# Kernel tuning notes

Measured on AMD Instinct MI355X. Metric: run time of the kernel, lower is better.

Reference implementation:

```python
import jax, jax.numpy as jnp
import numpy as np

B, N, D, Y = 4, 2048, 512, 8921


def setup_inputs() -> dict:
    key = jax.random.key(0)
    ks = jax.random.split(key, 9)
    scale = 1.0 / np.sqrt(D)
    return {
        "x": jax.random.normal(ks[0], (B, N, D), jnp.float32),
        "target": (jax.random.uniform(ks[1], (B, Y), jnp.float32) > 0.98).astype(jnp.float32),
        "y_flow": jax.random.normal(ks[2], (B, Y), jnp.float32),
        "U_w": jax.random.normal(ks[3], (Y, D), jnp.float32) * scale,
        "Ug_w": jax.random.normal(ks[4], (Y, D), jnp.float32) * scale,
        "final_w": jax.random.normal(ks[5], (Y, D), jnp.float32) * scale,
        "final_b": jax.random.normal(ks[6], (Y,), jnp.float32) * scale,
        "gate_w": jax.random.normal(ks[7], (D,), jnp.float32) * scale,
        "gate_b": jax.random.normal(ks[8], (), jnp.float32) * scale,
    }


def reference(x, target, y_flow, U_w, Ug_w, final_w, final_b, gate_w, gate_b):
    # Label attention branch: alpha = softmax(U_w @ x^T) over tokens -> [B, Y, N]
    alpha = jax.nn.softmax(jnp.einsum("yd,bnd->byn", U_w, x), axis=-1)
    m = jnp.einsum("byn,bnd->byd", alpha, x)  # [B, Y, D]

    # Gate attention branch
    alpha_g = jax.nn.softmax(jnp.einsum("yd,bnd->byn", Ug_w, x), axis=-1)
    m_g = jnp.einsum("byn,bnd->byd", alpha_g, x)  # [B, Y, D]

    # gate = tanh(Linear(D,1)(m_gate)) -> [B, Y]
    gate = jnp.tanh(jnp.einsum("byd,d->by", m_g, gate_w) + gate_b)

    # y = sum_d(final_w * m) + final_b + y_flow * gate
    y = jnp.einsum("yd,byd->by", final_w, m) + final_b + y_flow * gate

    # BCEWithLogitsLoss (mean): logaddexp(0, y) - y * target, numerically stable
    loss = jnp.mean(jnp.logaddexp(0.0, y) - y * target)
    return (y, loss)
```

## Files before the change

### kernel.cpp

```cpp
#include <hip/hip_runtime.h>
#include <stdint.h>

#define BQ 4
#define NQ 2048
#define DQ 512
#define YQ 8921
#define YGRP 140
#define NH 4
#define NCHQ 32
#define NUNITS (YGRP * BQ * NH)
#define NLP 140
#define GXOFF 65536
#define L2E 1.44269504088896340736f

typedef __attribute__((ext_vector_type(8))) short bf16x8;
typedef __attribute__((ext_vector_type(4))) float f32x4;

__device__ inline short f2bf(float f) {
  unsigned u = __float_as_uint(f);
  u += 0x7fffu + ((u >> 16) & 1u);
  return (short)(u >> 16);
}

__device__ inline bf16x8 pack8(float4 a, float4 b) {
  bf16x8 h;
  h[0] = f2bf(a.x); h[1] = f2bf(a.y); h[2] = f2bf(a.z); h[3] = f2bf(a.w);
  h[4] = f2bf(b.x); h[5] = f2bf(b.y); h[6] = f2bf(b.z); h[7] = f2bf(b.w);
  return h;
}

__device__ inline void gl_lds16(const void* g, void* l) {
  __builtin_amdgcn_global_load_lds((const __attribute__((address_space(1))) void*)g,
                                   (__attribute__((address_space(3))) void*)l, 16, 0, 0);
}

__global__ __launch_bounds__(256) void prep_gx(const float* __restrict__ x,
                                               const float* __restrict__ gate_w,
                                               float* __restrict__ gx) {
  int rid = blockIdx.x * 4 + (threadIdx.x >> 6);
  int lane = threadIdx.x & 63;
  const float* src = x + (size_t)rid * DQ + lane * 8;
  float4 v0 = *(const float4*)src;
  float4 v1 = *(const float4*)(src + 4);
  const float* gwp = gate_w + lane * 8;
  float s = v0.x * gwp[0] + v0.y * gwp[1] + v0.z * gwp[2] + v0.w * gwp[3]
          + v1.x * gwp[4] + v1.y * gwp[5] + v1.z * gwp[6] + v1.w * gwp[7];
#pragma unroll
  for (int d = 1; d < 64; d <<= 1) s += __shfl_xor(s, d);
  if (lane == 0) gx[rid] = s;
}

__global__ __launch_bounds__(256) void prep_xfrag(const float* __restrict__ x,
                                                  const float* __restrict__ gate_w,
                                                  char* __restrict__ ws_x2,
                                                  float* __restrict__ gx) {
  __shared__ float xs[16 * 512];
  int t = blockIdx.x;
  const float* src = x + ((size_t)t << 13);
  int tid = threadIdx.x;
#pragma unroll
  for (int i = 0; i < 8; ++i)
    *(float4*)(xs + i * 1024 + tid * 4) = *(const float4*)(src + i * 1024 + tid * 4);
  __syncthreads();
  char* dst = ws_x2 + ((size_t)t << 14);
#pragma unroll
  for (int i = 0; i < 4; ++i) {
    int s = i * 256 + tid;
    int l = s & 63, kk = s >> 6;
    int row = l & 15, g = l >> 4;
    const float* p = xs + row * 512 + kk * 32 + g * 8;
    *(bf16x8*)(dst + s * 16) = pack8(*(const float4*)p, *(const float4*)(p + 4));
  }
  int row = tid >> 4, sub = tid & 15;
  const float* xr = xs + row * 512 + sub * 32;
  const float* gw = gate_w + sub * 32;
  float s = 0.f;
#pragma unroll
  for (int i = 0; i < 8; ++i) {
    float4 a = *(const float4*)(xr + i * 4);
    float4 g = *(const float4*)(gw + i * 4);
    s += a.x * g.x + a.y * g.y + a.z * g.z + a.w * g.w;
  }
  s += __shfl_xor(s, 1); s += __shfl_xor(s, 2);
  s += __shfl_xor(s, 4); s += __shfl_xor(s, 8);
  if (sub == 0) gx[t * 16 + row] = s;
}

__global__ __launch_bounds__(256) void prep_w(const float* __restrict__ Uw,
                                              const float* __restrict__ Gw,
                                              const float* __restrict__ Fw,
                                              char* __restrict__ ws_w) {
  int rid = blockIdx.x * 4 + (threadIdx.x >> 6);
  if (rid >= 3 * YQ) return;
  int lane = threadIdx.x & 63;
  int mat = rid / YQ, y = rid % YQ;
  const float* src = (mat == 0 ? Uw : (mat == 1 ? Gw : Fw)) + (size_t)y * DQ + lane * 8;
  *(bf16x8*)(ws_w + (size_t)rid * 1024 + lane * 16) =
      pack8(*(const float4*)src, *(const float4*)(src + 4));
}

template<bool FULL>
__global__ __launch_bounds__(256, 2) void fused_kernel(
    const float* __restrict__ x, const char* __restrict__ ws_x2,
    const char* __restrict__ ws_w,
    const float* __restrict__ Uw, const float* __restrict__ Gw,
    const float* __restrict__ Fw, const float* __restrict__ gx,
    float4* __restrict__ ws_state) {
  extern __shared__ char smem[];
  const int tid = threadIdx.x, l = tid & 63, w = tid >> 6;
  const int lr = l & 15, lg4 = l >> 4;
  int u = (blockIdx.x & 7) * (NUNITS / 8) + (blockIdx.x >> 3);
  const int b = u / (YGRP * NH);
  const int r0 = u % (YGRP * NH);
  const int yg = r0 / NH, nh = r0 % NH;
  const int ybase = yg * 64 + w * 16;
  const int nbase = nh * (NQ / NH);

  bf16x8 wU[16], wG[16], wF[16];
  {
    int y = ybase + lr; if (y >= YQ) y = YQ - 1;
    if constexpr (FULL) {
      const char* p0 = ws_w + ((size_t)y * DQ + lg4 * 8) * 2;
#pragma unroll
      for (int kk = 0; kk < 16; ++kk) {
        wU[kk] = *(const bf16x8*)(p0 + kk * 64);
        wG[kk] = *(const bf16x8*)(p0 + (size_t)YQ * 1024 + kk * 64);
        wF[kk] = *(const bf16x8*)(p0 + (size_t)YQ * 2048 + kk * 64);
      }
    } else {
      const float* pu = Uw + (size_t)y * DQ + lg4 * 8;
      const float* pg = Gw + (size_t)y * DQ + lg4 * 8;
      const float* pf = Fw + (size_t)y * DQ + lg4 * 8;
#pragma unroll
      for (int kk = 0; kk < 16; ++kk) {
        wU[kk] = pack8(*(const float4*)(pu + kk * 32), *(const float4*)(pu + kk * 32 + 4));
        wG[kk] = pack8(*(const float4*)(pg + kk * 32), *(const float4*)(pg + kk * 32 + 4));
        wF[kk] = pack8(*(const float4*)(pf + kk * 32), *(const float4*)(pf + kk * 32 + 4));
      }
    }
  }

  float lU = 0.f, aU = 0.f, lG = 0.f, aG = 0.f;

  if constexpr (FULL) {
    *(float2*)(smem + GXOFF + tid * 8) = *(const float2*)(gx + b * NQ + nbase + tid * 2);
    const char* xb = ws_x2 + (((size_t)(b * 128 + nh * 32)) << 14);
    auto stage = [&](int c) {
      const char* src = xb + ((size_t)c << 14);
      char* lb = smem + (c & 3) * 16384;
#pragma unroll
      for (int j = 0; j < 4; ++j) {
        int s = w * 4 + j;
        gl_lds16(src + s * 1024 + l * 16, lb + s * 1024);
      }
    };
    auto mfma_only = [&](int c, f32x4& sU, f32x4& sG, f32x4& sF) {
      const char* ab = smem + (c & 3) * 16384 + l * 16;
#pragma unroll
      for (int r = 0; r < 4; ++r) { sU[r] = 0.f; sG[r] = 0.f; sF[r] = 0.f; }
      __builtin_amdgcn_s_setprio(1);
#pragma unroll
      for (int kk = 0; kk < 16; ++kk) {
        bf16x8 a = *(const bf16x8*)(ab + kk * 1024);
        sU = __builtin_amdgcn_mfma_f32_16x16x32_bf16(a, wU[kk], sU, 0, 0, 0);
        sG = __builtin_amdgcn_mfma_f32_16x16x32_bf16(a, wG[kk], sG, 0, 0, 0);
        sF = __builtin_amdgcn_mfma_f32_16x16x32_bf16(a, wF[kk], sF, 0, 0, 0);
      }
      __builtin_amdgcn_s_setprio(0);
    };
    auto tail = [&](int c, const f32x4& sU, const f32x4& sG, const f32x4& sF) {
      float4 gxv = *(const float4*)(smem + GXOFF + c * 64 + lg4 * 16);
      float gv[4] = {gxv.x, gxv.y, gxv.z, gxv.w};
#pragma unroll
      for (int r = 0; r < 4; ++r) {
        float eu = __builtin_amdgcn_exp2f(sU[r] * L2E);
        lU += eu; aU = fmaf(eu, sF[r], aU);
        float eg = __builtin_amdgcn_exp2f(sG[r] * L2E);
        lG += eg; aG = fmaf(eg, gv[r], aG);
      }
    };

    __syncthreads();
    stage(0); stage(1);
    asm volatile("s_waitcnt vmcnt(4)" ::: "memory");
    __builtin_amdgcn_s_barrier();

    f32x4 pU, pG, pF, qU, qG, qF;
    mfma_only(0, pU, pG, pF);

#pragma unroll 1
    for (int cp = 0; cp < 15; ++cp) {
      const int c0 = 2 * cp;
      stage(c0 + 2); stage(c0 + 3);
      asm volatile("s_waitcnt vmcnt(8)" ::: "memory");
      __builtin_amdgcn_sched_barrier(0);
      __builtin_amdgcn_s_barrier();
      mfma_only(c0 + 1, qU, qG, qF);
      tail(c0, pU, pG, pF);
      asm volatile("s_waitcnt vmcnt(4)" ::: "memory");
      __builtin_amdgcn_sched_barrier(0);
      __builtin_amdgcn_s_barrier();
      mfma_only(c0 + 2, pU, pG, pF);
      tail(c0 + 1, qU, qG, qF);
    }
    asm volatile("s_waitcnt vmcnt(0)" ::: "memory");
    __builtin_amdgcn_sched_barrier(0);
    __builtin_amdgcn_s_barrier();
    mfma_only(31, qU, qG, qF);
    tail(30, pU, pG, pF);
    tail(31, qU, qG, qF);
  } else {
    const float* gxb = gx + b * NQ + nbase + lg4 * 4;
    for (int c = 0; c < NCHQ; ++c) {
      __syncthreads();
#pragma unroll
      for (int j = 0; j < 4; ++j) {
        int slot = j * 256 + tid;
        int kk = slot >> 6, l2 = slot & 63;
        int row = l2 & 15, g4 = l2 >> 4;
        const float* g = x + ((size_t)(b * NQ + nbase + c * 16 + row)) * DQ
                       + kk * 32 + g4 * 8;
        *(bf16x8*)(smem + slot * 16) = pack8(*(const float4*)g, *(const float4*)(g + 4));
      }
      __syncthreads();
      const char* ab = smem + l * 16;
      f32x4 sU = {0.f, 0.f, 0.f, 0.f}, sG = sU, sF = sU;
#pragma unroll
      for (int kk = 0; kk < 16; ++kk) {
        bf16x8 a = *(const bf16x8*)(ab + kk * 1024);
        sU = __builtin_amdgcn_mfma_f32_16x16x32_bf16(a, wU[kk], sU, 0, 0, 0);
        sG = __builtin_amdgcn_mfma_f32_16x16x32_bf16(a, wG[kk], sG, 0, 0, 0);
        sF = __builtin_amdgcn_mfma_f32_16x16x32_bf16(a, wF[kk], sF, 0, 0, 0);
      }
      float4 gxv = *(const float4*)(gxb + c * 16);
      float gv[4] = {gxv.x, gxv.y, gxv.z, gxv.w};
#pragma unroll
      for (int r = 0; r < 4; ++r) {
        float eu = __builtin_amdgcn_exp2f(sU[r] * L2E);
        lU += eu; aU = fmaf(eu, sF[r], aU);
        float eg = __builtin_amdgcn_exp2f(sG[r] * L2E);
        lG += eg; aG = fmaf(eg, gv[r], aG);
      }
    }
  }

#pragma unroll
  for (int d = 16; d < 64; d <<= 1) {
    lU += __shfl_xor(lU, d); aU += __shfl_xor(aU, d);
    lG += __shfl_xor(lG, d); aG += __shfl_xor(aG, d);
  }

  int y = ybase + lr;
  if (lg4 == 0 && y < YQ) {
    float4 st; st.x = lU; st.y = aU; st.z = lG; st.w = aG;
    ws_state[(size_t)(b * NH + nh) * YQ + y] = st;
  }
}

__global__ __launch_bounds__(256) void merge_kernel(
    const float4* __restrict__ ws_state, const float* __restrict__ fb,
    const float* __restrict__ gate_b, const float* __restrict__ yflow,
    const float* __restrict__ target, float* __restrict__ out_y,
    float* __restrict__ loss_part) {
  __shared__ float sb[256];
  int t = blockIdx.x * 256 + threadIdx.x;
  float lt = 0.f;
  if (t < BQ * YQ) {
    int b = t / YQ, y = t % YQ;
    float lU = 0.f, aU = 0.f, lG = 0.f, aG = 0.f;
#pragma unroll
    for (int nh = 0; nh < NH; ++nh) {
      float4 s = ws_state[(size_t)(b * NH + nh) * YQ + y];
      lU += s.x; aU += s.y; lG += s.z; aG += s.w;
    }
    float gate = tanhf(aG / lG + gate_b[0]);
    float yv = aU / lU + fb[y] + yflow[t] * gate;
    out_y[t] = yv;
    float tg = target[t];
    lt = fmaxf(yv, 0.f) + log1pf(__expf(-fabsf(yv))) - yv * tg;
  }
  sb[threadIdx.x] = lt;
  __syncthreads();
  for (int st = 128; st > 0; st >>= 1) {
    if (threadIdx.x < st) sb[threadIdx.x] += sb[threadIdx.x + st];
    __syncthreads();
  }
  if (threadIdx.x == 0) loss_part[blockIdx.x] = sb[0];
}

__global__ __launch_bounds__(256) void loss_kernel(const float* __restrict__ lp,
                                                   float* __restrict__ out) {
  __shared__ float sb[256];
  float s = (threadIdx.x < NLP) ? lp[threadIdx.x] : 0.f;
  sb[threadIdx.x] = s;
  __syncthreads();
  for (int st = 128; st > 0; st >>= 1) {
    if (threadIdx.x < st) sb[threadIdx.x] += sb[threadIdx.x + st];
    __syncthreads();
  }
  if (threadIdx.x == 0) out[BQ * YQ] = sb[0] / (float)(BQ * YQ);
}

extern "C" void kernel_launch(void* const* d_in, const int* in_sizes, int n_in,
                              void* d_out, int out_size, void* d_ws, size_t ws_size,
                              hipStream_t stream) {
  const float* x      = (const float*)d_in[0];
  const float* target = (const float*)d_in[1];
  const float* yflow  = (const float*)d_in[2];
  const float* Uw     = (const float*)d_in[3];
  const float* Gw     = (const float*)d_in[4];
  const float* Fw     = (const float*)d_in[5];
  const float* fb     = (const float*)d_in[6];
  const float* gw     = (const float*)d_in[7];
  const float* gb     = (const float*)d_in[8];
  float* out = (float*)d_out;
  char* ws = (char*)d_ws;

  const size_t xbytes  = (size_t)BQ * NQ * DQ * 2;
  const size_t wbytes  = (size_t)3 * YQ * DQ * 2;
  const size_t gxbytes = (size_t)BQ * NQ * 4;
  const size_t stbytes = (size_t)BQ * NH * YQ * 16;
  const size_t lpbytes = (size_t)NLP * 4;
  const bool full = ws_size >= xbytes + wbytes + gxbytes + stbytes + lpbytes;

  char* ws_x2; char* ws_w; float* gxp; float4* stp; float* lp;
  if (full) {
    ws_x2 = ws; ws_w = ws + xbytes;
    gxp = (float*)(ws + xbytes + wbytes);
    stp = (float4*)(ws + xbytes + wbytes + gxbytes);
    lp  = (float*)(ws + xbytes + wbytes + gxbytes + stbytes);
  } else {
    ws_x2 = nullptr; ws_w = nullptr;
    gxp = (float*)ws;
    stp = (float4*)(ws + gxbytes);
    lp  = (float*)(ws + gxbytes + stbytes);
  }

  (void)hipFuncSetAttribute(reinterpret_cast<const void*>(&fused_kernel<true>),
                            hipFuncAttributeMaxDynamicSharedMemorySize, 67584);
  (void)hipFuncSetAttribute(reinterpret_cast<const void*>(&fused_kernel<false>),
                            hipFuncAttributeMaxDynamicSharedMemorySize, 16384);

  if (full) {
    prep_xfrag<<<dim3(BQ * 128), 256, 0, stream>>>(x, gw, ws_x2, gxp);
    prep_w<<<dim3((3 * YQ + 3) / 4), 256, 0, stream>>>(Uw, Gw, Fw, ws_w);
    fused_kernel<true ><<<dim3(NUNITS), 256, 67584, stream>>>(
        x, ws_x2, ws_w, Uw, Gw, Fw, gxp, stp);
  } else {
    prep_gx<<<dim3(2048), 256, 0, stream>>>(x, gw, gxp);
    fused_kernel<false><<<dim3(NUNITS), 256, 16384, stream>>>(
        x, ws_x2, ws_w, Uw, Gw, Fw, gxp, stp);
  }
  merge_kernel<<<dim3(NLP), 256, 0, stream>>>(stp, fb, gb, yflow, target, out, lp);
  loss_kernel<<<1, 256, 0, stream>>>(lp, out);
}
```

Before: 219.7 us.

## Split chunk MFMA into quarter phases with register double-buffered LDS reads, merge prep kernels

The main loop now processes each 16-token chunk in four k-quarters, holding LDS fragments in two register buffers so the reads for the next quarter overlap the current MFMAs. Global-to-LDS staging is spread one slice per quarter with finer waitcnt and barriers. The two prep kernels are merged into a single launch to save one kernel launch. In exchange the loop has more barriers per chunk and there is less overlap between the exp tail and the MFMAs, since tail now runs after the chunk's last MFMA instead of alongside the next chunk.

```diff
diff --git a/kernel.cpp b/kernel.cpp
--- a/kernel.cpp
+++ b/kernel.cpp
@@ -10,6 +10,7 @@
 #define NCHQ 32
 #define NUNITS (YGRP * BQ * NH)
 #define NLP 140
+#define NWB ((3 * YQ + 3) / 4)
 #define GXOFF 65536
 #define L2E 1.44269504088896340736f
 
@@ -50,53 +51,54 @@
   if (lane == 0) gx[rid] = s;
 }
 
-__global__ __launch_bounds__(256) void prep_xfrag(const float* __restrict__ x,
-                                                  const float* __restrict__ gate_w,
-                                                  char* __restrict__ ws_x2,
-                                                  float* __restrict__ gx) {
+__global__ __launch_bounds__(256) void prep_all(const float* __restrict__ x,
+                                                const float* __restrict__ gate_w,
+                                                const float* __restrict__ Uw,
+                                                const float* __restrict__ Gw,
+                                                const float* __restrict__ Fw,
+                                                char* __restrict__ ws_x2,
+                                                char* __restrict__ ws_w,
+                                                float* __restrict__ gx) {
   __shared__ float xs[16 * 512];
-  int t = blockIdx.x;
-  const float* src = x + ((size_t)t << 13);
   int tid = threadIdx.x;
-#pragma unroll
-  for (int i = 0; i < 8; ++i)
-    *(float4*)(xs + i * 1024 + tid * 4) = *(const float4*)(src + i * 1024 + tid * 4);
-  __syncthreads();
-  char* dst = ws_x2 + ((size_t)t << 14);
-#pragma unroll
-  for (int i = 0; i < 4; ++i) {
-    int s = i * 256 + tid;
-    int l = s & 63, kk = s >> 6;
-    int row = l & 15, g = l >> 4;
-    const float* p = xs + row * 512 + kk * 32 + g * 8;
-    *(bf16x8*)(dst + s * 16) = pack8(*(const float4*)p, *(const float4*)(p + 4));
-  }
-  int row = tid >> 4, sub = tid & 15;
-  const float* xr = xs + row * 512 + sub * 32;
-  const float* gw = gate_w + sub * 32;
-  float s = 0.f;
-#pragma unroll
-  for (int i = 0; i < 8; ++i) {
-    float4 a = *(const float4*)(xr + i * 4);
-    float4 g = *(const float4*)(gw + i * 4);
-    s += a.x * g.x + a.y * g.y + a.z * g.z + a.w * g.w;
-  }
-  s += __shfl_xor(s, 1); s += __shfl_xor(s, 2);
-  s += __shfl_xor(s, 4); s += __shfl_xor(s, 8);
-  if (sub == 0) gx[t * 16 + row] = s;
-}
-
-__global__ __launch_bounds__(256) void prep_w(const float* __restrict__ Uw,
-                                              const float* __restrict__ Gw,
-                                              const float* __restrict__ Fw,
-                                              char* __restrict__ ws_w) {
-  int rid = blockIdx.x * 4 + (threadIdx.x >> 6);
-  if (rid >= 3 * YQ) return;
-  int lane = threadIdx.x & 63;
-  int mat = rid / YQ, y = rid % YQ;
-  const float* src = (mat == 0 ? Uw : (mat == 1 ? Gw : Fw)) + (size_t)y * DQ + lane * 8;
-  *(bf16x8*)(ws_w + (size_t)rid * 1024 + lane * 16) =
-      pack8(*(const float4*)src, *(const float4*)(src + 4));
+  if (blockIdx.x < 512) {
+    int t = blockIdx.x;
+    const float* src = x + ((size_t)t << 13);
+#pragma unroll
+    for (int i = 0; i < 8; ++i)
+      *(float4*)(xs + i * 1024 + tid * 4) = *(const float4*)(src + i * 1024 + tid * 4);
+    __syncthreads();
+    char* dst = ws_x2 + ((size_t)t << 14);
+#pragma unroll
+    for (int i = 0; i < 4; ++i) {
+      int s = i * 256 + tid;
+      int l = s & 63, kk = s >> 6;
+      int row = l & 15, g = l >> 4;
+      const float* p = xs + row * 512 + kk * 32 + g * 8;
+      *(bf16x8*)(dst + s * 16) = pack8(*(const float4*)p, *(const float4*)(p + 4));
+    }
+    int row = tid >> 4, sub = tid & 15;
+    const float* xr = xs + row * 512 + sub * 32;
+    const float* gw = gate_w + sub * 32;
+    float s = 0.f;
+#pragma unroll
+    for (int i = 0; i < 8; ++i) {
+      float4 a = *(const float4*)(xr + i * 4);
+      float4 g = *(const float4*)(gw + i * 4);
+      s += a.x * g.x + a.y * g.y + a.z * g.z + a.w * g.w;
+    }
+    s += __shfl_xor(s, 1); s += __shfl_xor(s, 2);
+    s += __shfl_xor(s, 4); s += __shfl_xor(s, 8);
+    if (sub == 0) gx[t * 16 + row] = s;
+  } else {
+    int rid = (blockIdx.x - 512) * 4 + (tid >> 6);
+    if (rid >= 3 * YQ) return;
+    int lane = tid & 63;
+    int mat = rid / YQ, y = rid % YQ;
+    const float* src = (mat == 0 ? Uw : (mat == 1 ? Gw : Fw)) + (size_t)y * DQ + lane * 8;
+    *(bf16x8*)(ws_w + (size_t)rid * 1024 + lane * 16) =
+        pack8(*(const float4*)src, *(const float4*)(src + 4));
+  }
 }
 
 template<bool FULL>
@@ -145,30 +147,31 @@
   if constexpr (FULL) {
     *(float2*)(smem + GXOFF + tid * 8) = *(const float2*)(gx + b * NQ + nbase + tid * 2);
     const char* xb = ws_x2 + (((size_t)(b * 128 + nh * 32)) << 14);
-    auto stage = [&](int c) {
-      const char* src = xb + ((size_t)c << 14);
-      char* lb = smem + (c & 3) * 16384;
-#pragma unroll
-      for (int j = 0; j < 4; ++j) {
-        int s = w * 4 + j;
-        gl_lds16(src + s * 1024 + l * 16, lb + s * 1024);
-      }
+
+    f32x4 sU, sG, sF;
+    auto stage1 = [&](int c, int j) {
+      int s = w * 4 + j;
+      gl_lds16(xb + ((size_t)c << 14) + s * 1024 + l * 16,
+               smem + (c & 3) * 16384 + s * 1024);
     };
-    auto mfma_only = [&](int c, f32x4& sU, f32x4& sG, f32x4& sF) {
-      const char* ab = smem + (c & 3) * 16384 + l * 16;
-#pragma unroll
-      for (int r = 0; r < 4; ++r) { sU[r] = 0.f; sG[r] = 0.f; sF[r] = 0.f; }
+    auto read4 = [&](int c, int p, bf16x8* A) {
+      const char* ab = smem + (c & 3) * 16384 + p * 4096 + l * 16;
+      A[0] = *(const bf16x8*)(ab);
+      A[1] = *(const bf16x8*)(ab + 1024);
+      A[2] = *(const bf16x8*)(ab + 2048);
+      A[3] = *(const bf16x8*)(ab + 3072);
+    };
+    auto mfma12 = [&](const bf16x8* A, int p) {
       __builtin_amdgcn_s_setprio(1);
 #pragma unroll
-      for (int kk = 0; kk < 16; ++kk) {
-        bf16x8 a = *(const bf16x8*)(ab + kk * 1024);
-        sU = __builtin_amdgcn_mfma_f32_16x16x32_bf16(a, wU[kk], sU, 0, 0, 0);
-        sG = __builtin_amdgcn_mfma_f32_16x16x32_bf16(a, wG[kk], sG, 0, 0, 0);
-        sF = __builtin_amdgcn_mfma_f32_16x16x32_bf16(a, wF[kk], sF, 0, 0, 0);
+      for (int kk = 0; kk < 4; ++kk) {
+        sU = __builtin_amdgcn_mfma_f32_16x16x32_bf16(A[kk], wU[p * 4 + kk], sU, 0, 0, 0);
+        sG = __builtin_amdgcn_mfma_f32_16x16x32_bf16(A[kk], wG[p * 4 + kk], sG, 0, 0, 0);
+        sF = __builtin_amdgcn_mfma_f32_16x16x32_bf16(A[kk], wF[p * 4 + kk], sF, 0, 0, 0);
       }
       __builtin_amdgcn_s_setprio(0);
     };
-    auto tail = [&](int c, const f32x4& sU, const f32x4& sG, const f32x4& sF) {
+    auto tail = [&](int c) {
       float4 gxv = *(const float4*)(smem + GXOFF + c * 64 + lg4 * 16);
       float gv[4] = {gxv.x, gxv.y, gxv.z, gxv.w};
 #pragma unroll
@@ -181,34 +184,49 @@
     };
 
     __syncthreads();
-    stage(0); stage(1);
+#pragma unroll
+    for (int j = 0; j < 4; ++j) stage1(0, j);
+#pragma unroll
+    for (int j = 0; j < 4; ++j) stage1(1, j);
     asm volatile("s_waitcnt vmcnt(4)" ::: "memory");
     __builtin_amdgcn_s_barrier();
 
-    f32x4 pU, pG, pF, qU, qG, qF;
-    mfma_only(0, pU, pG, pF);
+    bf16x8 Ra[4], Rb[4];
+    read4(0, 0, Ra);
 
 #pragma unroll 1
-    for (int cp = 0; cp < 15; ++cp) {
-      const int c0 = 2 * cp;
-      stage(c0 + 2); stage(c0 + 3);
-      asm volatile("s_waitcnt vmcnt(8)" ::: "memory");
+    for (int c = 0; c < NCHQ; ++c) {
+      const int cn = (c + 1 < NCHQ) ? c + 1 : c;
+      const bool st = (c + 2 < NCHQ);
+#pragma unroll
+      for (int r = 0; r < 4; ++r) { sU[r] = 0.f; sG[r] = 0.f; sF[r] = 0.f; }
+      read4(c, 1, Rb);
+      if (st) stage1(c + 2, 0);
+      __builtin_amdgcn_s_barrier();
       __builtin_amdgcn_sched_barrier(0);
+      mfma12(Ra, 0);
+      read4(c, 2, Ra);
+      if (st) stage1(c + 2, 1);
       __builtin_amdgcn_s_barrier();
-      mfma_only(c0 + 1, qU, qG, qF);
-      tail(c0, pU, pG, pF);
-      asm volatile("s_waitcnt vmcnt(4)" ::: "memory");
       __builtin_amdgcn_sched_barrier(0);
+      mfma12(Rb, 1);
+      read4(c, 3, Rb);
+      if (st) {
+        stage1(c + 2, 2);
+        asm volatile("s_waitcnt vmcnt(3)" ::: "memory");
+      } else {
+        asm volatile("s_waitcnt vmcnt(0)" ::: "memory");
+      }
       __builtin_amdgcn_s_barrier();
-      mfma_only(c0 + 2, pU, pG, pF);
-      tail(c0 + 1, qU, qG, qF);
-    }
-    asm volatile("s_waitcnt vmcnt(0)" ::: "memory");
-    __builtin_amdgcn_sched_barrier(0);
-    __builtin_amdgcn_s_barrier();
-    mfma_only(31, qU, qG, qF);
-    tail(30, pU, pG, pF);
-    tail(31, qU, qG, qF);
+      __builtin_amdgcn_sched_barrier(0);
+      mfma12(Ra, 2);
+      read4(cn, 0, Ra);
+      if (st) stage1(c + 2, 3);
+      __builtin_amdgcn_s_barrier();
+      __builtin_amdgcn_sched_barrier(0);
+      mfma12(Rb, 3);
+      tail(c);
+    }
   } else {
     const float* gxb = gx + b * NQ + nbase + lg4 * 4;
     for (int c = 0; c < NCHQ; ++c) {
@@ -342,8 +360,7 @@
                             hipFuncAttributeMaxDynamicSharedMemorySize, 16384);
 
   if (full) {
-    prep_xfrag<<<dim3(BQ * 128), 256, 0, stream>>>(x, gw, ws_x2, gxp);
-    prep_w<<<dim3((3 * YQ + 3) / 4), 256, 0, stream>>>(Uw, Gw, Fw, ws_w);
+    prep_all<<<dim3(512 + NWB), 256, 0, stream>>>(x, gw, Uw, Gw, Fw, ws_x2, ws_w, gxp);
     fused_kernel<true ><<<dim3(NUNITS), 256, 67584, stream>>>(
         x, ws_x2, ws_w, Uw, Gw, Fw, gxp, stp);
   } else {
```

New measurement: 222.5 us. Within noise of the previous version (+1.3%).

## Split fused kernel into U/F and gate warp roles with 6 waves per block

Applied to the files above, without the earlier changes.

The fused attention kernel now runs 384 threads per block. Four waves hold U and F weight fragments and two waves hold G weights for 32 labels each, so each wave keeps two weight sets in registers instead of three. The software-pipelined 2-chunk loop becomes a simpler triple-buffered loop with one barrier per chunk, which also shrinks shared memory. The two prep kernels are merged into one launch, and the per-label state is split into two float2 arrays. Register pressure drops and more waves are resident, but the pipeline is simpler, there is one barrier per chunk, and work is uneven across wave roles.

```diff
diff --git a/kernel.cpp b/kernel.cpp
--- a/kernel.cpp
+++ b/kernel.cpp
@@ -10,7 +10,8 @@
 #define NCHQ 32
 #define NUNITS (YGRP * BQ * NH)
 #define NLP 140
-#define GXOFF 65536
+#define NWB ((3 * YQ + 3) / 4)
+#define GXOFF 49152
 #define L2E 1.44269504088896340736f
 
 typedef __attribute__((ext_vector_type(8))) short bf16x8;
@@ -50,62 +51,63 @@
   if (lane == 0) gx[rid] = s;
 }
 
-__global__ __launch_bounds__(256) void prep_xfrag(const float* __restrict__ x,
-                                                  const float* __restrict__ gate_w,
-                                                  char* __restrict__ ws_x2,
-                                                  float* __restrict__ gx) {
+__global__ __launch_bounds__(256) void prep_all(const float* __restrict__ x,
+                                                const float* __restrict__ gate_w,
+                                                const float* __restrict__ Uw,
+                                                const float* __restrict__ Gw,
+                                                const float* __restrict__ Fw,
+                                                char* __restrict__ ws_x2,
+                                                char* __restrict__ ws_w,
+                                                float* __restrict__ gx) {
   __shared__ float xs[16 * 512];
-  int t = blockIdx.x;
-  const float* src = x + ((size_t)t << 13);
   int tid = threadIdx.x;
-#pragma unroll
-  for (int i = 0; i < 8; ++i)
-    *(float4*)(xs + i * 1024 + tid * 4) = *(const float4*)(src + i * 1024 + tid * 4);
-  __syncthreads();
-  char* dst = ws_x2 + ((size_t)t << 14);
-#pragma unroll
-  for (int i = 0; i < 4; ++i) {
-    int s = i * 256 + tid;
-    int l = s & 63, kk = s >> 6;
-    int row = l & 15, g = l >> 4;
-    const float* p = xs + row * 512 + kk * 32 + g * 8;
-    *(bf16x8*)(dst + s * 16) = pack8(*(const float4*)p, *(const float4*)(p + 4));
-  }
-  int row = tid >> 4, sub = tid & 15;
-  const float* xr = xs + row * 512 + sub * 32;
-  const float* gw = gate_w + sub * 32;
-  float s = 0.f;
-#pragma unroll
-  for (int i = 0; i < 8; ++i) {
-    float4 a = *(const float4*)(xr + i * 4);
-    float4 g = *(const float4*)(gw + i * 4);
-    s += a.x * g.x + a.y * g.y + a.z * g.z + a.w * g.w;
-  }
-  s += __shfl_xor(s, 1); s += __shfl_xor(s, 2);
-  s += __shfl_xor(s, 4); s += __shfl_xor(s, 8);
-  if (sub == 0) gx[t * 16 + row] = s;
-}
-
-__global__ __launch_bounds__(256) void prep_w(const float* __restrict__ Uw,
-                                              const float* __restrict__ Gw,
-                                              const float* __restrict__ Fw,
-                                              char* __restrict__ ws_w) {
-  int rid = blockIdx.x * 4 + (threadIdx.x >> 6);
-  if (rid >= 3 * YQ) return;
-  int lane = threadIdx.x & 63;
-  int mat = rid / YQ, y = rid % YQ;
-  const float* src = (mat == 0 ? Uw : (mat == 1 ? Gw : Fw)) + (size_t)y * DQ + lane * 8;
-  *(bf16x8*)(ws_w + (size_t)rid * 1024 + lane * 16) =
-      pack8(*(const float4*)src, *(const float4*)(src + 4));
+  if (blockIdx.x < 512) {
+    int t = blockIdx.x;
+    const float* src = x + ((size_t)t << 13);
+#pragma unroll
+    for (int i = 0; i < 8; ++i)
+      *(float4*)(xs + i * 1024 + tid * 4) = *(const float4*)(src + i * 1024 + tid * 4);
+    __syncthreads();
+    char* dst = ws_x2 + ((size_t)t << 14);
+#pragma unroll
+    for (int i = 0; i < 4; ++i) {
+      int s = i * 256 + tid;
+      int l = s & 63, kk = s >> 6;
+      int row = l & 15, g = l >> 4;
+      const float* p = xs + row * 512 + kk * 32 + g * 8;
+      *(bf16x8*)(dst + s * 16) = pack8(*(const float4*)p, *(const float4*)(p + 4));
+    }
+    int row = tid >> 4, sub = tid & 15;
+    const float* xr = xs + row * 512 + sub * 32;
+    const float* gw = gate_w + sub * 32;
+    float s = 0.f;
+#pragma unroll
+    for (int i = 0; i < 8; ++i) {
+      float4 a = *(const float4*)(xr + i * 4);
+      float4 g = *(const float4*)(gw + i * 4);
+      s += a.x * g.x + a.y * g.y + a.z * g.z + a.w * g.w;
+    }
+    s += __shfl_xor(s, 1); s += __shfl_xor(s, 2);
+    s += __shfl_xor(s, 4); s += __shfl_xor(s, 8);
+    if (sub == 0) gx[t * 16 + row] = s;
+  } else {
+    int rid = (blockIdx.x - 512) * 4 + (tid >> 6);
+    if (rid >= 3 * YQ) return;
+    int lane = tid & 63;
+    int mat = rid / YQ, y = rid % YQ;
+    const float* src = (mat == 0 ? Uw : (mat == 1 ? Gw : Fw)) + (size_t)y * DQ + lane * 8;
+    *(bf16x8*)(ws_w + (size_t)rid * 1024 + lane * 16) =
+        pack8(*(const float4*)src, *(const float4*)(src + 4));
+  }
 }
 
 template<bool FULL>
-__global__ __launch_bounds__(256, 2) void fused_kernel(
+__global__ __launch_bounds__(384, 2) void fused_kernel(
     const float* __restrict__ x, const char* __restrict__ ws_x2,
     const char* __restrict__ ws_w,
     const float* __restrict__ Uw, const float* __restrict__ Gw,
     const float* __restrict__ Fw, const float* __restrict__ gx,
-    float4* __restrict__ ws_state) {
+    float2* __restrict__ stUF, float2* __restrict__ stG) {
   extern __shared__ char smem[];
   const int tid = threadIdx.x, l = tid & 63, w = tid >> 6;
   const int lr = l & 15, lg4 = l >> 4;
@@ -113,155 +115,168 @@
   const int b = u / (YGRP * NH);
   const int r0 = u % (YGRP * NH);
   const int yg = r0 / NH, nh = r0 % NH;
-  const int ybase = yg * 64 + w * 16;
   const int nbase = nh * (NQ / NH);
-
-  bf16x8 wU[16], wG[16], wF[16];
+  const bool isUF = (w < 4);
+  const int ya0 = yg * 64 + (isUF ? w * 16 : (w - 4) * 32);
+  const int yb0 = isUF ? ya0 : (ya0 + 16);
+
+  bf16x8 wA[16], wB[16];
   {
-    int y = ybase + lr; if (y >= YQ) y = YQ - 1;
+    int ya = ya0 + lr; if (ya >= YQ) ya = YQ - 1;
+    int yb = yb0 + lr; if (yb >= YQ) yb = YQ - 1;
     if constexpr (FULL) {
-      const char* p0 = ws_w + ((size_t)y * DQ + lg4 * 8) * 2;
+      const size_t yoff = (size_t)YQ * 1024;
+      const char* pa = ws_w + ((size_t)ya * DQ + lg4 * 8) * 2 + (isUF ? 0 : yoff);
+      const char* pb = ws_w + ((size_t)yb * DQ + lg4 * 8) * 2 + (isUF ? 2 * yoff : yoff);
 #pragma unroll
       for (int kk = 0; kk < 16; ++kk) {
-        wU[kk] = *(const bf16x8*)(p0 + kk * 64);
-        wG[kk] = *(const bf16x8*)(p0 + (size_t)YQ * 1024 + kk * 64);
-        wF[kk] = *(const bf16x8*)(p0 + (size_t)YQ * 2048 + kk * 64);
+        wA[kk] = *(const bf16x8*)(pa + kk * 64);
+        wB[kk] = *(const bf16x8*)(pb + kk * 64);
       }
     } else {
-      const float* pu = Uw + (size_t)y * DQ + lg4 * 8;
-      const float* pg = Gw + (size_t)y * DQ + lg4 * 8;
-      const float* pf = Fw + (size_t)y * DQ + lg4 * 8;
+      const float* pa = (isUF ? Uw : Gw) + (size_t)ya * DQ + lg4 * 8;
+      const float* pb = (isUF ? Fw : Gw) + (size_t)yb * DQ + lg4 * 8;
 #pragma unroll
       for (int kk = 0; kk < 16; ++kk) {
-        wU[kk] = pack8(*(const float4*)(pu + kk * 32), *(const float4*)(pu + kk * 32 + 4));
-        wG[kk] = pack8(*(const float4*)(pg + kk * 32), *(const float4*)(pg + kk * 32 + 4));
-        wF[kk] = pack8(*(const float4*)(pf + kk * 32), *(const float4*)(pf + kk * 32 + 4));
-      }
-    }
-  }
-
-  float lU = 0.f, aU = 0.f, lG = 0.f, aG = 0.f;
+        wA[kk] = pack8(*(const float4*)(pa + kk * 32), *(const float4*)(pa + kk * 32 + 4));
+        wB[kk] = pack8(*(const float4*)(pb + kk * 32), *(const float4*)(pb + kk * 32 + 4));
+      }
+    }
+  }
+
+  float l0 = 0.f, a0 = 0.f, l1 = 0.f, a1 = 0.f;
 
   if constexpr (FULL) {
-    *(float2*)(smem + GXOFF + tid * 8) = *(const float2*)(gx + b * NQ + nbase + tid * 2);
+    if (tid < 256)
+      *(float2*)(smem + GXOFF + tid * 8) = *(const float2*)(gx + b * NQ + nbase + tid * 2);
     const char* xb = ws_x2 + (((size_t)(b * 128 + nh * 32)) << 14);
     auto stage = [&](int c) {
       const char* src = xb + ((size_t)c << 14);
-      char* lb = smem + (c & 3) * 16384;
+      char* lb = smem + (c % 3) * 16384;
 #pragma unroll
       for (int j = 0; j < 4; ++j) {
         int s = w * 4 + j;
         gl_lds16(src + s * 1024 + l * 16, lb + s * 1024);
       }
     };
-    auto mfma_only = [&](int c, f32x4& sU, f32x4& sG, f32x4& sF) {
-      const char* ab = smem + (c & 3) * 16384 + l * 16;
-#pragma unroll
-      for (int r = 0; r < 4; ++r) { sU[r] = 0.f; sG[r] = 0.f; sF[r] = 0.f; }
+    auto compute = [&](int c) {
+      const char* ab = smem + (c % 3) * 16384 + l * 16;
+      f32x4 sA = {0.f, 0.f, 0.f, 0.f}, sB = sA;
       __builtin_amdgcn_s_setprio(1);
 #pragma unroll
       for (int kk = 0; kk < 16; ++kk) {
         bf16x8 a = *(const bf16x8*)(ab + kk * 1024);
-        sU = __builtin_amdgcn_mfma_f32_16x16x32_bf16(a, wU[kk], sU, 0, 0, 0);
-        sG = __builtin_amdgcn_mfma_f32_16x16x32_bf16(a, wG[kk], sG, 0, 0, 0);
-        sF = __builtin_amdgcn_mfma_f32_16x16x32_bf16(a, wF[kk], sF, 0, 0, 0);
+        sA = __builtin_amdgcn_mfma_f32_16x16x32_bf16(a, wA[kk], sA, 0, 0, 0);
+        sB = __builtin_amdgcn_mfma_f32_16x16x32_bf16(a, wB[kk], sB, 0, 0, 0);
       }
       __builtin_amdgcn_s_setprio(0);
+      if (isUF) {
+#pragma unroll
+        for (int r = 0; r < 4; ++r) {
+          float e = __builtin_amdgcn_exp2f(sA[r] * L2E);
+          l0 += e; a0 = fmaf(e, sB[r], a0);
+        }
+      } else {
+        float4 gxv = *(const float4*)(smem + GXOFF + c * 64 + lg4 * 16);
+        float gv[4] = {gxv.x, gxv.y, gxv.z, gxv.w};
+#pragma unroll
+        for (int r = 0; r < 4; ++r) {
+          float ea = __builtin_amdgcn_exp2f(sA[r] * L2E);
+          l0 += ea; a0 = fmaf(ea, gv[r], a0);
+          float eb = __builtin_amdgcn_exp2f(sB[r] * L2E);
+          l1 += eb; a1 = fmaf(eb, gv[r], a1);
+        }
+      }
     };
-    auto tail = [&](int c, const f32x4& sU, const f32x4& sG, const f32x4& sF) {
-      float4 gxv = *(const float4*)(smem + GXOFF + c * 64 + lg4 * 16);
-      float gv[4] = {gxv.x, gxv.y, gxv.z, gxv.w};
-#pragma unroll
-      for (int r = 0; r < 4; ++r) {
-        float eu = __builtin_amdgcn_exp2f(sU[r] * L2E);
-        lU += eu; aU = fmaf(eu, sF[r], aU);
-        float eg = __builtin_amdgcn_exp2f(sG[r] * L2E);
-        lG += eg; aG = fmaf(eg, gv[r], aG);
-      }
-    };
 
     __syncthreads();
-    stage(0); stage(1);
-    asm volatile("s_waitcnt vmcnt(4)" ::: "memory");
+    if (isUF) {
+      stage(0); stage(1);
+      asm volatile("s_waitcnt vmcnt(4)" ::: "memory");
+    }
     __builtin_amdgcn_s_barrier();
 
-    f32x4 pU, pG, pF, qU, qG, qF;
-    mfma_only(0, pU, pG, pF);
-
 #pragma unroll 1
-    for (int cp = 0; cp < 15; ++cp) {
-      const int c0 = 2 * cp;
-      stage(c0 + 2); stage(c0 + 3);
-      asm volatile("s_waitcnt vmcnt(8)" ::: "memory");
-      __builtin_amdgcn_sched_barrier(0);
-      __builtin_amdgcn_s_barrier();
-      mfma_only(c0 + 1, qU, qG, qF);
-      tail(c0, pU, pG, pF);
-      asm volatile("s_waitcnt vmcnt(4)" ::: "memory");
-      __builtin_amdgcn_sched_barrier(0);
-      __builtin_amdgcn_s_barrier();
-      mfma_only(c0 + 2, pU, pG, pF);
-      tail(c0 + 1, qU, qG, qF);
-    }
-    asm volatile("s_waitcnt vmcnt(0)" ::: "memory");
-    __builtin_amdgcn_sched_barrier(0);
-    __builtin_amdgcn_s_barrier();
-    mfma_only(31, qU, qG, qF);
-    tail(30, pU, pG, pF);
-    tail(31, qU, qG, qF);
+    for (int c = 0; c < NCHQ; ++c) {
+      if (isUF && c + 2 < NCHQ) stage(c + 2);
+      compute(c);
+      if (isUF) {
+        if (c + 2 < NCHQ)      asm volatile("s_waitcnt vmcnt(4)" ::: "memory");
+        else if (c + 1 < NCHQ) asm volatile("s_waitcnt vmcnt(0)" ::: "memory");
+      }
+      if (c + 1 < NCHQ) {
+        __builtin_amdgcn_sched_barrier(0);
+        __builtin_amdgcn_s_barrier();
+      }
+    }
   } else {
     const float* gxb = gx + b * NQ + nbase + lg4 * 4;
     for (int c = 0; c < NCHQ; ++c) {
       __syncthreads();
 #pragma unroll
-      for (int j = 0; j < 4; ++j) {
-        int slot = j * 256 + tid;
-        int kk = slot >> 6, l2 = slot & 63;
-        int row = l2 & 15, g4 = l2 >> 4;
-        const float* g = x + ((size_t)(b * NQ + nbase + c * 16 + row)) * DQ
-                       + kk * 32 + g4 * 8;
-        *(bf16x8*)(smem + slot * 16) = pack8(*(const float4*)g, *(const float4*)(g + 4));
+      for (int i = 0; i < 3; ++i) {
+        int slot = i * 384 + tid;
+        if (slot < 1024) {
+          int kk = slot >> 6, l2 = slot & 63;
+          int row = l2 & 15, g4 = l2 >> 4;
+          const float* g = x + ((size_t)(b * NQ + nbase + c * 16 + row)) * DQ
+                         + kk * 32 + g4 * 8;
+          *(bf16x8*)(smem + slot * 16) = pack8(*(const float4*)g, *(const float4*)(g + 4));
+        }
       }
       __syncthreads();
       const char* ab = smem + l * 16;
-      f32x4 sU = {0.f, 0.f, 0.f, 0.f}, sG = sU, sF = sU;
+      f32x4 sA = {0.f, 0.f, 0.f, 0.f}, sB = sA;
 #pragma unroll
       for (int kk = 0; kk < 16; ++kk) {
         bf16x8 a = *(const bf16x8*)(ab + kk * 1024);
-        sU = __builtin_amdgcn_mfma_f32_16x16x32_bf16(a, wU[kk], sU, 0, 0, 0);
-        sG = __builtin_amdgcn_mfma_f32_16x16x32_bf16(a, wG[kk], sG, 0, 0, 0);
-        sF = __builtin_amdgcn_mfma_f32_16x16x32_bf16(a, wF[kk], sF, 0, 0, 0);
-      }
-      float4 gxv = *(const float4*)(gxb + c * 16);
-      float gv[4] = {gxv.x, gxv.y, gxv.z, gxv.w};
-#pragma unroll
-      for (int r = 0; r < 4; ++r) {
-        float eu = __builtin_amdgcn_exp2f(sU[r] * L2E);
-        lU += eu; aU = fmaf(eu, sF[r], aU);
-        float eg = __builtin_amdgcn_exp2f(sG[r] * L2E);
-        lG += eg; aG = fmaf(eg, gv[r], aG);
+        sA = __builtin_amdgcn_mfma_f32_16x16x32_bf16(a, wA[kk], sA, 0, 0, 0);
+        sB = __builtin_amdgcn_mfma_f32_16x16x32_bf16(a, wB[kk], sB, 0, 0, 0);
+      }
+      if (isUF) {
+#pragma unroll
+        for (int r = 0; r < 4; ++r) {
+          float e = __builtin_amdgcn_exp2f(sA[r] * L2E);
+          l0 += e; a0 = fmaf(e, sB[r], a0);
+        }
+      } else {
+        float4 gxv = *(const float4*)(gxb + c * 16);
+        float gv[4] = {gxv.x, gxv.y, gxv.z, gxv.w};
+#pragma unroll
+        for (int r = 0; r < 4; ++r) {
+          float ea = __builtin_amdgcn_exp2f(sA[r] * L2E);
+          l0 += ea; a0 = fmaf(ea, gv[r], a0);
+          float eb = __builtin_amdgcn_exp2f(sB[r] * L2E);
+          l1 += eb; a1 = fmaf(eb, gv[r], a1);
+        }
       }
     }
   }
 
 #pragma unroll
   for (int d = 16; d < 64; d <<= 1) {
-    lU += __shfl_xor(lU, d); aU += __shfl_xor(aU, d);
-    lG += __shfl_xor(lG, d); aG += __shfl_xor(aG, d);
-  }
-
-  int y = ybase + lr;
-  if (lg4 == 0 && y < YQ) {
-    float4 st; st.x = lU; st.y = aU; st.z = lG; st.w = aG;
-    ws_state[(size_t)(b * NH + nh) * YQ + y] = st;
+    l0 += __shfl_xor(l0, d); a0 += __shfl_xor(a0, d);
+    l1 += __shfl_xor(l1, d); a1 += __shfl_xor(a1, d);
+  }
+
+  if (lg4 == 0) {
+    const size_t base = (size_t)(b * NH + nh) * YQ;
+    if (isUF) {
+      int y = ya0 + lr;
+      if (y < YQ) { float2 s; s.x = l0; s.y = a0; stUF[base + y] = s; }
+    } else {
+      int ya = ya0 + lr, yb = yb0 + lr;
+      if (ya < YQ) { float2 s; s.x = l0; s.y = a0; stG[base + ya] = s; }
+      if (yb < YQ) { float2 s; s.x = l1; s.y = a1; stG[base + yb] = s; }
+    }
   }
 }
 
 __global__ __launch_bounds__(256) void merge_kernel(
-    const float4* __restrict__ ws_state, const float* __restrict__ fb,
-    const float* __restrict__ gate_b, const float* __restrict__ yflow,
-    const float* __restrict__ target, float* __restrict__ out_y,
-    float* __restrict__ loss_part) {
+    const float2* __restrict__ stUF, const float2* __restrict__ stG,
+    const float* __restrict__ fb, const float* __restrict__ gate_b,
+    const float* __restrict__ yflow, const float* __restrict__ target,
+    float* __restrict__ out_y, float* __restrict__ loss_part) {
   __shared__ float sb[256];
   int t = blockIdx.x * 256 + threadIdx.x;
   float lt = 0.f;
@@ -270,8 +285,9 @@
     float lU = 0.f, aU = 0.f, lG = 0.f, aG = 0.f;
 #pragma unroll
     for (int nh = 0; nh < NH; ++nh) {
-      float4 s = ws_state[(size_t)(b * NH + nh) * YQ + y];
-      lU += s.x; aU += s.y; lG += s.z; aG += s.w;
+      float2 s1 = stUF[(size_t)(b * NH + nh) * YQ + y];
+      float2 s2 = stG[(size_t)(b * NH + nh) * YQ + y];
+      lU += s1.x; aU += s1.y; lG += s2.x; aG += s2.y;
     }
     float gate = tanhf(aG / lG + gate_b[0]);
     float yv = aU / lU + fb[y] + yflow[t] * gate;
@@ -319,38 +335,39 @@
   const size_t xbytes  = (size_t)BQ * NQ * DQ * 2;
   const size_t wbytes  = (size_t)3 * YQ * DQ * 2;
   const size_t gxbytes = (size_t)BQ * NQ * 4;
-  const size_t stbytes = (size_t)BQ * NH * YQ * 16;
+  const size_t stbytes = (size_t)BQ * NH * YQ * 8;
   const size_t lpbytes = (size_t)NLP * 4;
-  const bool full = ws_size >= xbytes + wbytes + gxbytes + stbytes + lpbytes;
-
-  char* ws_x2; char* ws_w; float* gxp; float4* stp; float* lp;
+  const bool full = ws_size >= xbytes + wbytes + gxbytes + 2 * stbytes + lpbytes;
+
+  char* ws_x2; char* ws_w; float* gxp; float2* s1p; float2* s2p; float* lp;
   if (full) {
     ws_x2 = ws; ws_w = ws + xbytes;
     gxp = (float*)(ws + xbytes + wbytes);
-    stp = (float4*)(ws + xbytes + wbytes + gxbytes);
-    lp  = (float*)(ws + xbytes + wbytes + gxbytes + stbytes);
+    s1p = (float2*)(ws + xbytes + wbytes + gxbytes);
+    s2p = (float2*)(ws + xbytes + wbytes + gxbytes + stbytes);
+    lp  = (float*)(ws + xbytes + wbytes + gxbytes + 2 * stbytes);
   } else {
     ws_x2 = nullptr; ws_w = nullptr;
     gxp = (float*)ws;
-    stp = (float4*)(ws + gxbytes);
-    lp  = (float*)(ws + gxbytes + stbytes);
+    s1p = (float2*)(ws + gxbytes);
+    s2p = (float2*)(ws + gxbytes + stbytes);
+    lp  = (float*)(ws + gxbytes + 2 * stbytes);
   }
 
   (void)hipFuncSetAttribute(reinterpret_cast<const void*>(&fused_kernel<true>),
-                            hipFuncAttributeMaxDynamicSharedMemorySize, 67584);
+                            hipFuncAttributeMaxDynamicSharedMemorySize, 51200);
   (void)hipFuncSetAttribute(reinterpret_cast<const void*>(&fused_kernel<false>),
                             hipFuncAttributeMaxDynamicSharedMemorySize, 16384);
 
   if (full) {
-    prep_xfrag<<<dim3(BQ * 128), 256, 0, stream>>>(x, gw, ws_x2, gxp);
-    prep_w<<<dim3((3 * YQ + 3) / 4), 256, 0, stream>>>(Uw, Gw, Fw, ws_w);
-    fused_kernel<true ><<<dim3(NUNITS), 256, 67584, stream>>>(
-        x, ws_x2, ws_w, Uw, Gw, Fw, gxp, stp);
+    prep_all<<<dim3(512 + NWB), 256, 0, stream>>>(x, gw, Uw, Gw, Fw, ws_x2, ws_w, gxp);
+    fused_kernel<true ><<<dim3(NUNITS), 384, 51200, stream>>>(
+        x, ws_x2, ws_w, Uw, Gw, Fw, gxp, s1p, s2p);
   } else {
     prep_gx<<<dim3(2048), 256, 0, stream>>>(x, gw, gxp);
-    fused_kernel<false><<<dim3(NUNITS), 256, 16384, stream>>>(
-        x, ws_x2, ws_w, Uw, Gw, Fw, gxp, stp);
-  }
-  merge_kernel<<<dim3(NLP), 256, 0, stream>>>(stp, fb, gb, yflow, target, out, lp);
+    fused_kernel<false><<<dim3(NUNITS), 384, 16384, stream>>>(
+        x, ws_x2, ws_w, Uw, Gw, Fw, gxp, s1p, s2p);
+  }
+  merge_kernel<<<dim3(NLP), 256, 0, stream>>>(s1p, s2p, fb, gb, yflow, target, out, lp);
   loss_kernel<<<1, 256, 0, stream>>>(lp, out);
 }
```

Result: slower. 319.7 us (+45.5%).
